# Performance work log

Hardware: AMD Instinct MI355X
Metric: run time of the kernel (lower is better)

Reference implementation:

```python
import jax, jax.numpy as jnp
import numpy as np

N_NODES = 50000
N_EDGES = 800000
NODE_FEAT = 3
HID = 64
L = 4


def setup_inputs() -> dict:
    key = jax.random.key(0)
    ks = jax.random.split(key, 16)
    s = 0.05  # init scale
    inp = {
        'node_pos': jax.random.normal(ks[0], (N_NODES, 3), jnp.float32),
        'node_features': jax.random.normal(ks[1], (N_NODES, NODE_FEAT), jnp.float32),
        'edge_index': jax.random.randint(ks[2], (2, N_EDGES), 0, N_NODES, jnp.int64),
        # encoders
        'enc_w': jax.random.normal(ks[3], (NODE_FEAT, HID), jnp.float32) * s,
        'enc_b': jnp.zeros((HID,), jnp.float32),
        'edge_enc_w': jax.random.normal(ks[4], (3, HID), jnp.float32) * s,
        'edge_enc_b': jnp.zeros((HID,), jnp.float32),
        # stacked per-layer GNOLayer params
        'ew1': jax.random.normal(ks[5], (L, 3 * HID, HID), jnp.float32) * s,
        'eb1': jnp.zeros((L, HID), jnp.float32),
        'ew2': jax.random.normal(ks[6], (L, HID, HID), jnp.float32) * s,
        'eb2': jnp.zeros((L, HID), jnp.float32),
        'nw1': jax.random.normal(ks[7], (L, 2 * HID, HID), jnp.float32) * s,
        'nb1': jnp.zeros((L, HID), jnp.float32),
        'nw2': jax.random.normal(ks[8], (L, HID, HID), jnp.float32) * s,
        'nb2': jnp.zeros((L, HID), jnp.float32),
        # decoder
        'dec_w': jax.random.normal(ks[9], (HID, 1), jnp.float32) * s,
        'dec_b': jnp.zeros((1,), jnp.float32),
    }
    return inp


def reference(node_pos, node_features, edge_index, enc_w, enc_b, edge_enc_w,
              edge_enc_b, ew1, eb1, ew2, eb2, nw1, nb1, nw2, nb2, dec_w, dec_b):
    src, dst = edge_index[0], edge_index[1]
    edge_vec = node_pos[dst] - node_pos[src]            # [E, 3]
    h = node_features @ enc_w + enc_b                   # [N, H]
    e = edge_vec @ edge_enc_w + edge_enc_b              # [E, H]

    def layer(h, p):
        w1, b1, w2, b2, m1, c1, m2, c2 = p
        edge_in = jnp.concatenate([h[src], h[dst], e], axis=-1)   # [E, 3H]
        msg = jax.nn.relu(edge_in @ w1 + b1) @ w2 + b2            # [E, H]
        agg = jax.ops.segment_sum(msg, dst, num_segments=N_NODES)  # [N, H]
        node_in = jnp.concatenate([h, agg], axis=-1)              # [N, 2H]
        return jax.nn.relu(node_in @ m1 + c1) @ m2 + c2, None

    h, _ = jax.lax.scan(layer, h, (ew1, eb1, ew2, eb2, nw1, nb1, nw2, nb2))
    return h @ dec_w + dec_b                            # [N, 1]
```

## Files before the change

kernel.cpp:

```cpp
#include <hip/hip_runtime.h>

#define N_NODES 50000
#define N_EDGES 800000
#define HID 64
#define LAYERS 4
#define EP_NPB 28
#define EP_CAP 2048

typedef unsigned short u16;
typedef __attribute__((ext_vector_type(8))) __bf16 bf16x8;
typedef __attribute__((ext_vector_type(8))) unsigned short u16x8;
typedef __attribute__((ext_vector_type(4))) float f32x4;

__device__ __forceinline__ u16 f2bf(float f) {
  unsigned u = __builtin_bit_cast(unsigned, f);
  u += 0x7fffu + ((u >> 16) & 1u);
  return (u16)(u >> 16);
}
__device__ __forceinline__ float bf2f(u16 s) {
  return __builtin_bit_cast(float, ((unsigned)s) << 16);
}

__global__ __launch_bounds__(256) void init_kernel(
    const float* __restrict__ nf, const float* __restrict__ enc_w,
    const float* __restrict__ enc_b,
    const float* __restrict__ ew1, const float* __restrict__ eb1,
    const float* __restrict__ ew2, const float* __restrict__ eb2,
    const float* __restrict__ nw1, const float* __restrict__ nw2,
    const float* __restrict__ edge_enc_w, const float* __restrict__ edge_enc_b,
    u16* __restrict__ h, u16* W1abT, float* Wvx, float* b1x,
    u16* NB1T, float* bb2, u16* M2T, int* __restrict__ cnt) {
  const int T = gridDim.x * 256;
  int tid = blockIdx.x * 256 + threadIdx.x;
  for (int i = tid; i < N_NODES; i += T) cnt[i] = 0;
  {
    const int szA = LAYERS * 128 * 64, szV = LAYERS * 3 * 64, szB = LAYERS * 64;
    const int szN = LAYERS * 64 * 128, szb2 = LAYERS * 64, szM = LAYERS * 64 * 64;
    const int tot = szA + szV + szB + szN + szb2 + szM;
    for (int i = tid; i < tot; i += T) {
      int idx = i;
      if (idx < szA) {
        int l = idx / (128 * 64); int r = idx % (128 * 64);
        int nfc = r / 64; int k = r % 64;
        int half = nfc >> 6, f = nfc & 63;
        W1abT[idx] = f2bf(ew1[(l * 192 + half * 64 + k) * 64 + f]);
        continue;
      }
      idx -= szA;
      if (idx < szV) {
        int l = idx / 192, r = idx % 192, a = r / 64, f = r % 64;
        float s = 0.f;
        for (int m = 0; m < 64; ++m) s += edge_enc_w[a * 64 + m] * ew1[(l * 192 + 128 + m) * 64 + f];
        Wvx[idx] = s;
        continue;
      }
      idx -= szV;
      if (idx < szB) {
        int l = idx / 64, f = idx % 64;
        float s = eb1[l * 64 + f];
        for (int m = 0; m < 64; ++m) s += edge_enc_b[m] * ew1[(l * 192 + 128 + m) * 64 + f];
        b1x[idx] = s;
        continue;
      }
      idx -= szB;
      if (idx < szN) {
        int l = idx / 8192, r = idx % 8192, f = r / 128, k = r % 128;
        float v;
        if (k < 64) v = nw1[(l * 128 + k) * 64 + f];
        else {
          int j = k - 64; float s = 0.f;
          for (int g = 0; g < 64; ++g)
            s += ew2[(l * 64 + j) * 64 + g] * nw1[(l * 128 + 64 + g) * 64 + f];
          v = s;
        }
        NB1T[idx] = f2bf(v);
        continue;
      }
      idx -= szN;
      if (idx < szb2) {
        int l = idx / 64, f = idx % 64;
        float s = 0.f;
        for (int g = 0; g < 64; ++g) s += eb2[l * 64 + g] * nw1[(l * 128 + 64 + g) * 64 + f];
        bb2[idx] = s;
        continue;
      }
      idx -= szb2;
      int l = idx / 4096, r = idx % 4096, f = r / 64, k = r % 64;
      M2T[idx] = f2bf(nw2[(l * 64 + k) * 64 + f]);
    }
  }
  for (int i = tid; i < N_NODES * HID; i += T) {
    int n = i >> 6, j = i & 63;
    float s = enc_b[j]
            + nf[n * 3 + 0] * enc_w[j]
            + nf[n * 3 + 1] * enc_w[64 + j]
            + nf[n * 3 + 2] * enc_w[128 + j];
    h[i] = f2bf(s);
  }
}

__global__ __launch_bounds__(256) void hist_kernel(const int* __restrict__ dstA,
                                                   int* __restrict__ cnt,
                                                   int* __restrict__ rank) {
  int idx = blockIdx.x * 256 + threadIdx.x;
  if (idx < N_EDGES) rank[idx] = atomicAdd(&cnt[dstA[idx]], 1);
}

#define SCAN_NBLK 25
__global__ __launch_bounds__(256) void scan1_kernel(const int* __restrict__ cnt,
                                                    int* __restrict__ offs,
                                                    int* __restrict__ partials) {
  __shared__ int sm[2048];
  __shared__ int ws2[256];
  int t = threadIdx.x, b = blockIdx.x;
  int base = b * 2048;
#pragma unroll
  for (int i = 0; i < 8; ++i) {
    int idx = base + i * 256 + t;
    sm[i * 256 + t] = (idx < N_NODES) ? cnt[idx] : 0;
  }
  __syncthreads();
  int loc[8]; int s = 0;
#pragma unroll
  for (int i = 0; i < 8; ++i) { loc[i] = s; s += sm[t * 8 + i]; }
  ws2[t] = s;
  __syncthreads();
  for (int off = 1; off < 256; off <<= 1) {
    int u = (t >= off) ? ws2[t - off] : 0;
    __syncthreads();
    ws2[t] += u;
    __syncthreads();
  }
  int tbase = (t > 0) ? ws2[t - 1] : 0;
  if (t == 255) partials[b] = ws2[255];
#pragma unroll
  for (int i = 0; i < 8; ++i) {
    int idx = base + t * 8 + i;
    if (idx < N_NODES) offs[idx] = tbase + loc[i];
  }
}

__global__ __launch_bounds__(256) void scan3_kernel(int* __restrict__ offs,
                                                    const int* __restrict__ partials) {
  __shared__ int pref;
  int blk = (blockIdx.x * 256) >> 11;
  if (threadIdx.x == 0) {
    int s = 0;
    for (int i = 0; i < blk; ++i) s += partials[i];
    pref = s;
  }
  __syncthreads();
  int idx = blockIdx.x * 256 + threadIdx.x;
  if (idx < N_NODES) offs[idx] += pref;
}

__global__ __launch_bounds__(256) void scatter_kernel(const int* __restrict__ ei,
                                                      const int* __restrict__ offs,
                                                      const int* __restrict__ rank,
                                                      int* __restrict__ srcS64) {
  int idx = blockIdx.x * 256 + threadIdx.x;
  if (idx >= N_EDGES) return;
  int s = ei[idx], d = ei[N_EDGES + idx];
  srcS64[offs[d] + rank[idx]] = s << 6;
}

__global__ __launch_bounds__(256) void su_kernel(const u16* __restrict__ h,
                                                 const u16* __restrict__ W1abT,
                                                 const float* __restrict__ Wvx,
                                                 const float* __restrict__ b1x,
                                                 const float* __restrict__ pos,
                                                 u16* __restrict__ Sarr,
                                                 u16* __restrict__ Uarr, int layer) {
  __shared__ float sPos[192];
  int t = threadIdx.x;
  int lane = t & 63, wvi = t >> 6;
  int n16 = lane & 15, quad = lane >> 4;
  int n0 = blockIdx.x * 64;
  if (t < 192) {
    int idx = n0 * 3 + t;
    sPos[t] = (idx < N_NODES * 3) ? pos[idx] : 0.f;
  }
  __syncthreads();

  bf16x8 B[2][2];
  float w0[2], w1[2], w2[2], bb[2]; bool isU[2];
#pragma unroll
  for (int nt = 0; nt < 2; ++nt) {
    int col = wvi * 32 + nt * 16 + n16;
    const u16* p = W1abT + (size_t)(layer * 128 + col) * 64 + quad * 8;
    B[nt][0] = __builtin_bit_cast(bf16x8, *(const u16x8*)(p));
    B[nt][1] = __builtin_bit_cast(bf16x8, *(const u16x8*)(p + 32));
    int f = col & 63; isU[nt] = col >= 64;
    w0[nt] = Wvx[(layer * 3 + 0) * 64 + f];
    w1[nt] = Wvx[(layer * 3 + 1) * 64 + f];
    w2[nt] = Wvx[(layer * 3 + 2) * 64 + f];
    bb[nt] = b1x[layer * 64 + f];
  }
  f32x4 acc[4][2];
#pragma unroll
  for (int m = 0; m < 4; ++m)
#pragma unroll
    for (int nt = 0; nt < 2; ++nt) acc[m][nt] = (f32x4){0.f, 0.f, 0.f, 0.f};

#pragma unroll
  for (int m = 0; m < 4; ++m) {
    int row = n0 + m * 16 + n16;
    if (row >= N_NODES) row = N_NODES - 1;
    const u16* hp = h + (size_t)row * 64 + quad * 8;
    bf16x8 a0 = __builtin_bit_cast(bf16x8, *(const u16x8*)(hp));
    bf16x8 a1 = __builtin_bit_cast(bf16x8, *(const u16x8*)(hp + 32));
#pragma unroll
    for (int nt = 0; nt < 2; ++nt) {
      acc[m][nt] = __builtin_amdgcn_mfma_f32_16x16x32_bf16(a0, B[nt][0], acc[m][nt], 0, 0, 0);
      acc[m][nt] = __builtin_amdgcn_mfma_f32_16x16x32_bf16(a1, B[nt][1], acc[m][nt], 0, 0, 0);
    }
  }
#pragma unroll
  for (int m = 0; m < 4; ++m)
#pragma unroll
    for (int nt = 0; nt < 2; ++nt) {
      int col = wvi * 32 + nt * 16 + n16;
      int f = col & 63;
#pragma unroll
      for (int r = 0; r < 4; ++r) {
        int e = m * 16 + quad * 4 + r;
        int grow = n0 + e;
        if (grow < N_NODES) {
          float P = sPos[e * 3] * w0[nt] + sPos[e * 3 + 1] * w1[nt] + sPos[e * 3 + 2] * w2[nt];
          if (!isU[nt]) Sarr[(size_t)grow * 64 + f] = f2bf(acc[m][nt][r] - P);
          else          Uarr[(size_t)grow * 64 + f] = f2bf(acc[m][nt][r] + P + bb[nt]);
        }
      }
    }
}

__global__ __launch_bounds__(256) void ep_kernel(const u16* __restrict__ Sarr,
                                                 const u16* __restrict__ Uarr,
                                                 const int* __restrict__ srcS64,
                                                 const int* __restrict__ offs,
                                                 u16* __restrict__ aggH) {
  __shared__ int sIdx[EP_CAP];
  __shared__ int sOff[EP_NPB + 1];
  int t = threadIdx.x;
  int f = t & 63, wvi = t >> 6;
  int d0b = blockIdx.x * EP_NPB;
  if (t <= EP_NPB) {
    int d = d0b + t;
    sOff[t] = (d < N_NODES) ? offs[d] : N_EDGES;
  }
  __syncthreads();
  int eS = sOff[0];
  int nE = sOff[EP_NPB] - eS;
  bool fit = (nE <= EP_CAP);
  if (fit) {
    for (int i = t; i < nE; i += 256) sIdx[i] = srcS64[eS + i];
  }
  __syncthreads();

  for (int i = 0; i < 7; ++i) {
    int nl = wvi * 7 + i;
    int d = d0b + nl;
    if (d >= N_NODES) break;
    int e0 = sOff[nl];
    int deg = sOff[nl + 1] - e0;
    float Ub = bf2f(Uarr[(size_t)d * 64 + f]);
    float sum = 0.f;
    int full = deg & ~7;
    int base = 0;
    if (fit) {
      int rel = e0 - eS;
      for (; base < full; base += 8) {
        u16 S[8];
#pragma unroll
        for (int k = 0; k < 8; ++k) {
          int s64 = sIdx[rel + base + k];
          S[k] = Sarr[(size_t)s64 + f];
        }
#pragma unroll
        for (int k = 0; k < 8; ++k) sum += fmaxf(bf2f(S[k]) + Ub, 0.f);
      }
      if (base < deg) {
        u16 S[8]; bool ok[8];
#pragma unroll
        for (int k = 0; k < 8; ++k) {
          int j = base + k;
          ok[k] = j < deg;
          int s64 = sIdx[rel + (ok[k] ? j : 0)];
          S[k] = Sarr[(size_t)s64 + f];
        }
#pragma unroll
        for (int k = 0; k < 8; ++k) {
          float z = fmaxf(bf2f(S[k]) + Ub, 0.f);
          sum += ok[k] ? z : 0.f;
        }
      }
    } else {
      for (; base < full; base += 8) {
        u16 S[8];
#pragma unroll
        for (int k = 0; k < 8; ++k) {
          int s64 = srcS64[e0 + base + k];
          S[k] = Sarr[(size_t)s64 + f];
        }
#pragma unroll
        for (int k = 0; k < 8; ++k) sum += fmaxf(bf2f(S[k]) + Ub, 0.f);
      }
      if (base < deg) {
        u16 S[8]; bool ok[8];
#pragma unroll
        for (int k = 0; k < 8; ++k) {
          int j = base + k;
          ok[k] = j < deg;
          int s64 = srcS64[e0 + (ok[k] ? j : 0)];
          S[k] = Sarr[(size_t)s64 + f];
        }
#pragma unroll
        for (int k = 0; k < 8; ++k) {
          float z = fmaxf(bf2f(S[k]) + Ub, 0.f);
          sum += ok[k] ? z : 0.f;
        }
      }
    }
    aggH[(size_t)d * 64 + f] = f2bf(sum);
  }
}

__global__ __launch_bounds__(256) void node_kernel(
    const u16* __restrict__ h, const u16* __restrict__ aggH,
    const int* __restrict__ cnt,
    const u16* __restrict__ NB1T, const float* __restrict__ nb1,
    const float* __restrict__ bb2,
    const u16* __restrict__ M2T, const float* __restrict__ nb2,
    u16* __restrict__ h2, int layer,
    const u16* __restrict__ W1abT, const float* __restrict__ Wvx,
    const float* __restrict__ b1x, const float* __restrict__ pos,
    u16* __restrict__ Sarr, u16* __restrict__ Uarr,
    const float* __restrict__ dec_w, const float* __restrict__ dec_b,
    float* __restrict__ out) {
  __shared__ u16 Hs[64 * 72];
  __shared__ float sDeg[64];
  __shared__ float sPos[192];
  __shared__ float sRed[64][4];
  int t = threadIdx.x;
  int lane = t & 63, wvi = t >> 6;
  int n16 = lane & 15, quad = lane >> 4;
  int F = wvi * 16;
  int n0 = blockIdx.x * 64;

  if (t < 64) {
    int gn = n0 + t;
    sDeg[t] = (gn < N_NODES) ? (float)cnt[gn] : 0.f;
  }
  if (t >= 64 && t < 256) {
    int i = t - 64;
    int idx = n0 * 3 + i;
    sPos[i] = (idx < N_NODES * 3) ? pos[idx] : 0.f;
  }

  bf16x8 B1[4], B2[2];
  {
    const u16* p = NB1T + (size_t)(layer * 64 + F + n16) * 128 + quad * 8;
#pragma unroll
    for (int ks = 0; ks < 4; ++ks) B1[ks] = __builtin_bit_cast(bf16x8, *(const u16x8*)(p + ks * 32));
    const u16* q = M2T + (size_t)(layer * 64 + F + n16) * 64 + quad * 8;
#pragma unroll
    for (int ks = 0; ks < 2; ++ks) B2[ks] = __builtin_bit_cast(bf16x8, *(const u16x8*)(q + ks * 32));
  }
  float bias1 = nb1[layer * 64 + F + n16];
  float bb2f = bb2[layer * 64 + F + n16];
  float bias2 = nb2[layer * 64 + F + n16];
  __syncthreads();

  f32x4 acc[4];
#pragma unroll
  for (int m = 0; m < 4; ++m) acc[m] = (f32x4){0.f, 0.f, 0.f, 0.f};
#pragma unroll
  for (int m = 0; m < 4; ++m) {
    int row = n0 + m * 16 + n16;
    if (row >= N_NODES) row = N_NODES - 1;
    const u16* hp = h + (size_t)row * 64 + quad * 8;
    const u16* ap = aggH + (size_t)row * 64 + quad * 8;
    bf16x8 a0 = __builtin_bit_cast(bf16x8, *(const u16x8*)(hp));
    bf16x8 a1 = __builtin_bit_cast(bf16x8, *(const u16x8*)(hp + 32));
    bf16x8 a2 = __builtin_bit_cast(bf16x8, *(const u16x8*)(ap));
    bf16x8 a3 = __builtin_bit_cast(bf16x8, *(const u16x8*)(ap + 32));
    acc[m] = __builtin_amdgcn_mfma_f32_16x16x32_bf16(a0, B1[0], acc[m], 0, 0, 0);
    acc[m] = __builtin_amdgcn_mfma_f32_16x16x32_bf16(a1, B1[1], acc[m], 0, 0, 0);
    acc[m] = __builtin_amdgcn_mfma_f32_16x16x32_bf16(a2, B1[2], acc[m], 0, 0, 0);
    acc[m] = __builtin_amdgcn_mfma_f32_16x16x32_bf16(a3, B1[3], acc[m], 0, 0, 0);
  }
#pragma unroll
  for (int m = 0; m < 4; ++m)
#pragma unroll
    for (int r = 0; r < 4; ++r) {
      int e = m * 16 + quad * 4 + r;
      float v = acc[m][r] + bias1 + sDeg[e] * bb2f;
      v = v > 0.f ? v : 0.f;
      Hs[e * 72 + F + n16] = f2bf(v);
    }
  __syncthreads();

  float c2[4][4];
#pragma unroll
  for (int m = 0; m < 4; ++m) {
    const u16* hp = Hs + (m * 16 + n16) * 72 + quad * 8;
    f32x4 c = (f32x4){0.f, 0.f, 0.f, 0.f};
#pragma unroll
    for (int ks = 0; ks < 2; ++ks) {
      bf16x8 a = __builtin_bit_cast(bf16x8, *(const u16x8*)(hp + ks * 32));
      c = __builtin_amdgcn_mfma_f32_16x16x32_bf16(a, B2[ks], c, 0, 0, 0);
    }
#pragma unroll
    for (int r = 0; r < 4; ++r) c2[m][r] = c[r] + bias2;
  }
  __syncthreads();

#pragma unroll
  for (int m = 0; m < 4; ++m)
#pragma unroll
    for (int r = 0; r < 4; ++r) {
      int e = m * 16 + quad * 4 + r;
      u16 hv = f2bf(c2[m][r]);
      Hs[e * 72 + F + n16] = hv;
      int gn = n0 + e;
      if (layer < LAYERS - 1 && gn < N_NODES)
        h2[(size_t)gn * 64 + F + n16] = hv;
    }
  __syncthreads();

  if (layer < LAYERS - 1) {
    int lp = layer + 1;
    bf16x8 B3[2][2];
    float w0[2], w1[2], w2[2], bb[2]; bool isU[2];
#pragma unroll
    for (int nt = 0; nt < 2; ++nt) {
      int col = wvi * 32 + nt * 16 + n16;
      const u16* p = W1abT + (size_t)(lp * 128 + col) * 64 + quad * 8;
      B3[nt][0] = __builtin_bit_cast(bf16x8, *(const u16x8*)(p));
      B3[nt][1] = __builtin_bit_cast(bf16x8, *(const u16x8*)(p + 32));
      int f = col & 63; isU[nt] = col >= 64;
      w0[nt] = Wvx[(lp * 3 + 0) * 64 + f];
      w1[nt] = Wvx[(lp * 3 + 1) * 64 + f];
      w2[nt] = Wvx[(lp * 3 + 2) * 64 + f];
      bb[nt] = b1x[lp * 64 + f];
    }
    f32x4 a3[4][2];
#pragma unroll
    for (int m = 0; m < 4; ++m)
#pragma unroll
      for (int nt = 0; nt < 2; ++nt) a3[m][nt] = (f32x4){0.f, 0.f, 0.f, 0.f};
#pragma unroll
    for (int m = 0; m < 4; ++m) {
      const u16* hp = Hs + (m * 16 + n16) * 72 + quad * 8;
      bf16x8 a0 = __builtin_bit_cast(bf16x8, *(const u16x8*)(hp));
      bf16x8 a1 = __builtin_bit_cast(bf16x8, *(const u16x8*)(hp + 32));
#pragma unroll
      for (int nt = 0; nt < 2; ++nt) {
        a3[m][nt] = __builtin_amdgcn_mfma_f32_16x16x32_bf16(a0, B3[nt][0], a3[m][nt], 0, 0, 0);
        a3[m][nt] = __builtin_amdgcn_mfma_f32_16x16x32_bf16(a1, B3[nt][1], a3[m][nt], 0, 0, 0);
      }
    }
#pragma unroll
    for (int m = 0; m < 4; ++m)
#pragma unroll
      for (int nt = 0; nt < 2; ++nt) {
        int col = wvi * 32 + nt * 16 + n16;
        int f = col & 63;
#pragma unroll
        for (int r = 0; r < 4; ++r) {
          int e = m * 16 + quad * 4 + r;
          int grow = n0 + e;
          if (grow < N_NODES) {
            float P = sPos[e * 3] * w0[nt] + sPos[e * 3 + 1] * w1[nt] + sPos[e * 3 + 2] * w2[nt];
            if (!isU[nt]) Sarr[(size_t)grow * 64 + f] = f2bf(a3[m][nt][r] - P);
            else          Uarr[(size_t)grow * 64 + f] = f2bf(a3[m][nt][r] + P + bb[nt]);
          }
        }
      }
  } else {
    int e = t >> 2, part = t & 3;
    float s = 0.f;
#pragma unroll
    for (int j = 0; j < 16; ++j)
      s += bf2f(Hs[e * 72 + part * 16 + j]) * dec_w[part * 16 + j];
    sRed[e][part] = s;
    __syncthreads();
    if (part == 0) {
      int gn = n0 + e;
      if (gn < N_NODES)
        out[gn] = sRed[e][0] + sRed[e][1] + sRed[e][2] + sRed[e][3] + dec_b[0];
    }
  }
}

extern "C" void kernel_launch(void* const* d_in, const int* in_sizes, int n_in,
                              void* d_out, int out_size, void* d_ws, size_t ws_size,
                              hipStream_t stream) {
  const float* node_pos   = (const float*)d_in[0];
  const float* node_feat  = (const float*)d_in[1];
  const int*   edge_index = (const int*)d_in[2];
  const float* enc_w      = (const float*)d_in[3];
  const float* enc_b      = (const float*)d_in[4];
  const float* edge_enc_w = (const float*)d_in[5];
  const float* edge_enc_b = (const float*)d_in[6];
  const float* ew1        = (const float*)d_in[7];
  const float* eb1        = (const float*)d_in[8];
  const float* ew2        = (const float*)d_in[9];
  const float* eb2        = (const float*)d_in[10];
  const float* nw1        = (const float*)d_in[11];
  const float* nb1        = (const float*)d_in[12];
  const float* nw2        = (const float*)d_in[13];
  const float* nb2        = (const float*)d_in[14];
  const float* dec_w      = (const float*)d_in[15];
  const float* dec_b      = (const float*)d_in[16];
  float* out = (float*)d_out;

  char* ws = (char*)d_ws;
  size_t off = 0;
  u16*    hA    = (u16*)(ws + off);    off += (size_t)N_NODES * 64 * 2;
  u16*    hB    = (u16*)(ws + off);    off += (size_t)N_NODES * 64 * 2;
  u16*    Sarr  = (u16*)(ws + off);    off += (size_t)N_NODES * 64 * 2;
  u16*    Uarr  = (u16*)(ws + off);    off += (size_t)N_NODES * 64 * 2;
  u16*    aggH  = (u16*)(ws + off);    off += (size_t)N_NODES * 64 * 2;
  u16*    W1abT = (u16*)(ws + off);    off += (size_t)LAYERS * 128 * 64 * 2;
  float*  Wvx   = (float*)(ws + off);  off += (size_t)LAYERS * 3 * 64 * 4;
  float*  b1x   = (float*)(ws + off);  off += (size_t)LAYERS * 64 * 4;
  u16*    NB1T  = (u16*)(ws + off);    off += (size_t)LAYERS * 64 * 128 * 2;
  float*  bb2   = (float*)(ws + off);  off += (size_t)LAYERS * 64 * 4;
  u16*    M2T   = (u16*)(ws + off);    off += (size_t)LAYERS * 64 * 64 * 2;
  int*    cnt      = (int*)(ws + off); off += (size_t)N_NODES * 4;
  int*    offsB    = (int*)(ws + off); off += (size_t)N_NODES * 4;
  int*    partials = (int*)(ws + off); off += 32 * 4;
  int*    rank     = (int*)(ws + off); off += (size_t)N_EDGES * 4;
  int*    srcS64   = (int*)(ws + off); off += (size_t)N_EDGES * 4;

  const int* dstA = edge_index + N_EDGES;
  const int NBLK = (N_NODES + 63) / 64;
  const int EP_GRID = (N_NODES + EP_NPB - 1) / EP_NPB;

  init_kernel<<<1024, 256, 0, stream>>>(
      node_feat, enc_w, enc_b, ew1, eb1, ew2, eb2, nw1, nw2,
      edge_enc_w, edge_enc_b, hA, W1abT, Wvx, b1x, NB1T, bb2, M2T, cnt);

  hist_kernel<<<(N_EDGES + 255) / 256, 256, 0, stream>>>(dstA, cnt, rank);
  scan1_kernel<<<SCAN_NBLK, 256, 0, stream>>>(cnt, offsB, partials);
  scan3_kernel<<<(N_NODES + 255) / 256, 256, 0, stream>>>(offsB, partials);
  scatter_kernel<<<(N_EDGES + 255) / 256, 256, 0, stream>>>(edge_index, offsB, rank, srcS64);

  su_kernel<<<NBLK, 256, 0, stream>>>(hA, W1abT, Wvx, b1x, node_pos, Sarr, Uarr, 0);

  u16* hcur = hA; u16* hnext = hB;
  for (int l = 0; l < LAYERS; ++l) {
    ep_kernel<<<EP_GRID, 256, 0, stream>>>(Sarr, Uarr, srcS64, offsB, aggH);
    node_kernel<<<NBLK, 256, 0, stream>>>(hcur, aggH, cnt, NB1T, nb1, bb2, M2T, nb2,
                                          hnext, l, W1abT, Wvx, b1x, node_pos,
                                          Sarr, Uarr, dec_w, dec_b, out);
    u16* tmp = hcur; hcur = hnext; hnext = tmp;
  }
}
```

Measured before the change: 345.8 us.

## Split S table into feature halves and fuse scatter with first SU pass

The per-node S table is stored as two 32-feature halves, and the edge-gather kernel now runs two blocks per node group, one per half. Each wave processes two destination nodes with 32 lanes each, which shrinks the gathered working set per pass and is meant to improve cache hit rates on random source gathers. The scatter kernel and the first SU projection are merged into one launch to drop a kernel boundary. Costs: lane pairs with different degrees run the masked tail up to the larger degree, and the offsets and Uarr values are read twice.

```diff
diff --git a/kernel.cpp b/kernel.cpp
--- a/kernel.cpp
+++ b/kernel.cpp
@@ -4,7 +4,7 @@
 #define N_EDGES 800000
 #define HID 64
 #define LAYERS 4
-#define EP_NPB 28
+#define EP_NPB 32
 #define EP_CAP 2048
 
 typedef unsigned short u16;
@@ -154,28 +154,26 @@
   if (idx < N_NODES) offs[idx] += pref;
 }
 
-__global__ __launch_bounds__(256) void scatter_kernel(const int* __restrict__ ei,
-                                                      const int* __restrict__ offs,
-                                                      const int* __restrict__ rank,
-                                                      int* __restrict__ srcS64) {
-  int idx = blockIdx.x * 256 + threadIdx.x;
-  if (idx >= N_EDGES) return;
-  int s = ei[idx], d = ei[N_EDGES + idx];
-  srcS64[offs[d] + rank[idx]] = s << 6;
-}
-
-__global__ __launch_bounds__(256) void su_kernel(const u16* __restrict__ h,
-                                                 const u16* __restrict__ W1abT,
-                                                 const float* __restrict__ Wvx,
-                                                 const float* __restrict__ b1x,
-                                                 const float* __restrict__ pos,
-                                                 u16* __restrict__ Sarr,
-                                                 u16* __restrict__ Uarr, int layer) {
+#define SCAT_BLKS 3125
+__global__ __launch_bounds__(256) void scatter_su_kernel(
+    const int* __restrict__ ei, const int* __restrict__ offs,
+    const int* __restrict__ rank, int* __restrict__ srcS32,
+    const u16* __restrict__ h, const u16* __restrict__ W1abT,
+    const float* __restrict__ Wvx, const float* __restrict__ b1x,
+    const float* __restrict__ pos,
+    u16* __restrict__ S0, u16* __restrict__ S1, u16* __restrict__ Uarr) {
+  if (blockIdx.x < SCAT_BLKS) {
+    int idx = blockIdx.x * 256 + threadIdx.x;
+    if (idx >= N_EDGES) return;
+    int s = ei[idx], d = ei[N_EDGES + idx];
+    srcS32[offs[d] + rank[idx]] = s << 5;
+    return;
+  }
   __shared__ float sPos[192];
   int t = threadIdx.x;
   int lane = t & 63, wvi = t >> 6;
   int n16 = lane & 15, quad = lane >> 4;
-  int n0 = blockIdx.x * 64;
+  int n0 = (blockIdx.x - SCAT_BLKS) * 64;
   if (t < 192) {
     int idx = n0 * 3 + t;
     sPos[t] = (idx < N_NODES * 3) ? pos[idx] : 0.f;
@@ -187,14 +185,14 @@
 #pragma unroll
   for (int nt = 0; nt < 2; ++nt) {
     int col = wvi * 32 + nt * 16 + n16;
-    const u16* p = W1abT + (size_t)(layer * 128 + col) * 64 + quad * 8;
+    const u16* p = W1abT + (size_t)col * 64 + quad * 8;
     B[nt][0] = __builtin_bit_cast(bf16x8, *(const u16x8*)(p));
     B[nt][1] = __builtin_bit_cast(bf16x8, *(const u16x8*)(p + 32));
     int f = col & 63; isU[nt] = col >= 64;
-    w0[nt] = Wvx[(layer * 3 + 0) * 64 + f];
-    w1[nt] = Wvx[(layer * 3 + 1) * 64 + f];
-    w2[nt] = Wvx[(layer * 3 + 2) * 64 + f];
-    bb[nt] = b1x[layer * 64 + f];
+    w0[nt] = Wvx[0 * 64 + f];
+    w1[nt] = Wvx[1 * 64 + f];
+    w2[nt] = Wvx[2 * 64 + f];
+    bb[nt] = b1x[f];
   }
   f32x4 acc[4][2];
 #pragma unroll
@@ -227,23 +225,32 @@
         int grow = n0 + e;
         if (grow < N_NODES) {
           float P = sPos[e * 3] * w0[nt] + sPos[e * 3 + 1] * w1[nt] + sPos[e * 3 + 2] * w2[nt];
-          if (!isU[nt]) Sarr[(size_t)grow * 64 + f] = f2bf(acc[m][nt][r] - P);
-          else          Uarr[(size_t)grow * 64 + f] = f2bf(acc[m][nt][r] + P + bb[nt]);
-        }
-      }
-    }
-}
-
-__global__ __launch_bounds__(256) void ep_kernel(const u16* __restrict__ Sarr,
+          if (!isU[nt]) {
+            u16* Sh = (f < 32) ? S0 : S1;
+            Sh[(size_t)grow * 32 + (f & 31)] = f2bf(acc[m][nt][r] - P);
+          } else {
+            Uarr[(size_t)grow * 64 + f] = f2bf(acc[m][nt][r] + P + bb[nt]);
+          }
+        }
+      }
+    }
+}
+
+__global__ __launch_bounds__(256) void ep_kernel(const u16* __restrict__ S0,
+                                                 const u16* __restrict__ S1,
                                                  const u16* __restrict__ Uarr,
-                                                 const int* __restrict__ srcS64,
+                                                 const int* __restrict__ srcS32,
                                                  const int* __restrict__ offs,
                                                  u16* __restrict__ aggH) {
   __shared__ int sIdx[EP_CAP];
   __shared__ int sOff[EP_NPB + 1];
   int t = threadIdx.x;
-  int f = t & 63, wvi = t >> 6;
-  int d0b = blockIdx.x * EP_NPB;
+  int half = blockIdx.x & 1;
+  int nb = blockIdx.x >> 1;
+  const u16* Sh = half ? S1 : S0;
+  int lane = t & 63, wvi = t >> 6;
+  int f = lane & 31, pairSel = lane >> 5;
+  int d0b = nb * EP_NPB;
   if (t <= EP_NPB) {
     int d = d0b + t;
     sOff[t] = (d < N_NODES) ? offs[d] : N_EDGES;
@@ -253,40 +260,42 @@
   int nE = sOff[EP_NPB] - eS;
   bool fit = (nE <= EP_CAP);
   if (fit) {
-    for (int i = t; i < nE; i += 256) sIdx[i] = srcS64[eS + i];
-  }
-  __syncthreads();
-
-  for (int i = 0; i < 7; ++i) {
-    int nl = wvi * 7 + i;
+    for (int i = t; i < nE; i += 256) sIdx[i] = srcS32[eS + i];
+  }
+  __syncthreads();
+
+  for (int i = 0; i < EP_NPB / 8; ++i) {
+    int nl = wvi * 8 + i * 2 + pairSel;
     int d = d0b + nl;
-    if (d >= N_NODES) break;
-    int e0 = sOff[nl];
-    int deg = sOff[nl + 1] - e0;
-    float Ub = bf2f(Uarr[(size_t)d * 64 + f]);
+    bool valid = d < N_NODES;
+    int e0 = valid ? sOff[nl] : eS;
+    int deg = valid ? sOff[nl + 1] - e0 : 0;
+    float Ub = valid ? bf2f(Uarr[(size_t)d * 64 + half * 32 + f]) : 0.f;
     float sum = 0.f;
-    int full = deg & ~7;
+    int degO = __shfl_xor(deg, 32);
+    int fullC = (deg < degO ? deg : degO) & ~7;
+    int maxD = deg > degO ? deg : degO;
     int base = 0;
     if (fit) {
       int rel = e0 - eS;
-      for (; base < full; base += 8) {
+      for (; base < fullC; base += 8) {
         u16 S[8];
 #pragma unroll
         for (int k = 0; k < 8; ++k) {
-          int s64 = sIdx[rel + base + k];
-          S[k] = Sarr[(size_t)s64 + f];
+          int s32 = sIdx[rel + base + k];
+          S[k] = Sh[(size_t)s32 + f];
         }
 #pragma unroll
         for (int k = 0; k < 8; ++k) sum += fmaxf(bf2f(S[k]) + Ub, 0.f);
       }
-      if (base < deg) {
+      for (; base < maxD; base += 8) {
         u16 S[8]; bool ok[8];
 #pragma unroll
         for (int k = 0; k < 8; ++k) {
           int j = base + k;
           ok[k] = j < deg;
-          int s64 = sIdx[rel + (ok[k] ? j : 0)];
-          S[k] = Sarr[(size_t)s64 + f];
+          int s32 = sIdx[rel + (ok[k] ? j : 0)];
+          S[k] = Sh[(size_t)s32 + f];
         }
 #pragma unroll
         for (int k = 0; k < 8; ++k) {
@@ -295,24 +304,14 @@
         }
       }
     } else {
-      for (; base < full; base += 8) {
-        u16 S[8];
-#pragma unroll
-        for (int k = 0; k < 8; ++k) {
-          int s64 = srcS64[e0 + base + k];
-          S[k] = Sarr[(size_t)s64 + f];
-        }
-#pragma unroll
-        for (int k = 0; k < 8; ++k) sum += fmaxf(bf2f(S[k]) + Ub, 0.f);
-      }
-      if (base < deg) {
+      for (; base < maxD; base += 8) {
         u16 S[8]; bool ok[8];
 #pragma unroll
         for (int k = 0; k < 8; ++k) {
           int j = base + k;
           ok[k] = j < deg;
-          int s64 = srcS64[e0 + (ok[k] ? j : 0)];
-          S[k] = Sarr[(size_t)s64 + f];
+          int s32 = srcS32[e0 + (ok[k] ? j : 0)];
+          S[k] = Sh[(size_t)s32 + f];
         }
 #pragma unroll
         for (int k = 0; k < 8; ++k) {
@@ -321,7 +320,7 @@
         }
       }
     }
-    aggH[(size_t)d * 64 + f] = f2bf(sum);
+    if (valid) aggH[(size_t)d * 64 + half * 32 + f] = f2bf(sum);
   }
 }
 
@@ -334,7 +333,7 @@
     u16* __restrict__ h2, int layer,
     const u16* __restrict__ W1abT, const float* __restrict__ Wvx,
     const float* __restrict__ b1x, const float* __restrict__ pos,
-    u16* __restrict__ Sarr, u16* __restrict__ Uarr,
+    u16* __restrict__ S0, u16* __restrict__ S1, u16* __restrict__ Uarr,
     const float* __restrict__ dec_w, const float* __restrict__ dec_b,
     float* __restrict__ out) {
   __shared__ u16 Hs[64 * 72];
@@ -472,8 +471,12 @@
           int grow = n0 + e;
           if (grow < N_NODES) {
             float P = sPos[e * 3] * w0[nt] + sPos[e * 3 + 1] * w1[nt] + sPos[e * 3 + 2] * w2[nt];
-            if (!isU[nt]) Sarr[(size_t)grow * 64 + f] = f2bf(a3[m][nt][r] - P);
-            else          Uarr[(size_t)grow * 64 + f] = f2bf(a3[m][nt][r] + P + bb[nt]);
+            if (!isU[nt]) {
+              u16* Sh = (f < 32) ? S0 : S1;
+              Sh[(size_t)grow * 32 + (f & 31)] = f2bf(a3[m][nt][r] - P);
+            } else {
+              Uarr[(size_t)grow * 64 + f] = f2bf(a3[m][nt][r] + P + bb[nt]);
+            }
           }
         }
       }
@@ -519,7 +522,8 @@
   size_t off = 0;
   u16*    hA    = (u16*)(ws + off);    off += (size_t)N_NODES * 64 * 2;
   u16*    hB    = (u16*)(ws + off);    off += (size_t)N_NODES * 64 * 2;
-  u16*    Sarr  = (u16*)(ws + off);    off += (size_t)N_NODES * 64 * 2;
+  u16*    S0    = (u16*)(ws + off);    off += (size_t)N_NODES * 32 * 2;
+  u16*    S1    = (u16*)(ws + off);    off += (size_t)N_NODES * 32 * 2;
   u16*    Uarr  = (u16*)(ws + off);    off += (size_t)N_NODES * 64 * 2;
   u16*    aggH  = (u16*)(ws + off);    off += (size_t)N_NODES * 64 * 2;
   u16*    W1abT = (u16*)(ws + off);    off += (size_t)LAYERS * 128 * 64 * 2;
@@ -532,11 +536,11 @@
   int*    offsB    = (int*)(ws + off); off += (size_t)N_NODES * 4;
   int*    partials = (int*)(ws + off); off += 32 * 4;
   int*    rank     = (int*)(ws + off); off += (size_t)N_EDGES * 4;
-  int*    srcS64   = (int*)(ws + off); off += (size_t)N_EDGES * 4;
+  int*    srcS32   = (int*)(ws + off); off += (size_t)N_EDGES * 4;
 
   const int* dstA = edge_index + N_EDGES;
   const int NBLK = (N_NODES + 63) / 64;
-  const int EP_GRID = (N_NODES + EP_NPB - 1) / EP_NPB;
+  const int EP_GRID = 2 * ((N_NODES + EP_NPB - 1) / EP_NPB);
 
   init_kernel<<<1024, 256, 0, stream>>>(
       node_feat, enc_w, enc_b, ew1, eb1, ew2, eb2, nw1, nw2,
@@ -545,16 +549,16 @@
   hist_kernel<<<(N_EDGES + 255) / 256, 256, 0, stream>>>(dstA, cnt, rank);
   scan1_kernel<<<SCAN_NBLK, 256, 0, stream>>>(cnt, offsB, partials);
   scan3_kernel<<<(N_NODES + 255) / 256, 256, 0, stream>>>(offsB, partials);
-  scatter_kernel<<<(N_EDGES + 255) / 256, 256, 0, stream>>>(edge_index, offsB, rank, srcS64);
-
-  su_kernel<<<NBLK, 256, 0, stream>>>(hA, W1abT, Wvx, b1x, node_pos, Sarr, Uarr, 0);
+  scatter_su_kernel<<<SCAT_BLKS + NBLK, 256, 0, stream>>>(
+      edge_index, offsB, rank, srcS32,
+      hA, W1abT, Wvx, b1x, node_pos, S0, S1, Uarr);
 
   u16* hcur = hA; u16* hnext = hB;
   for (int l = 0; l < LAYERS; ++l) {
-    ep_kernel<<<EP_GRID, 256, 0, stream>>>(Sarr, Uarr, srcS64, offsB, aggH);
+    ep_kernel<<<EP_GRID, 256, 0, stream>>>(S0, S1, Uarr, srcS32, offsB, aggH);
     node_kernel<<<NBLK, 256, 0, stream>>>(hcur, aggH, cnt, NB1T, nb1, bb2, M2T, nb2,
                                           hnext, l, W1abT, Wvx, b1x, node_pos,
-                                          Sarr, Uarr, dec_w, dec_b, out);
+                                          S0, S1, Uarr, dec_w, dec_b, out);
     u16* tmp = hcur; hcur = hnext; hnext = tmp;
   }
 }
```

After: 347.2 us. No clear change (+0.4%).
